# Kernel tuning notes

Hardware: AMD Instinct MI355X
Metric: run time of the kernel (lower is better)

The kernel has to match this reference:

```python
import jax, jax.numpy as jnp
import numpy as np

N, E, D, O, STEP = 100000, 640000, 128, 64, 10


def setup_inputs() -> dict:
    key = jax.random.key(0)
    k1, k2, k3, k4, k5 = jax.random.split(key, 5)
    x = jax.random.normal(k1, (N, D), dtype=jnp.float32)
    edge_index = jax.random.randint(k2, (2, E), 0, N, dtype=jnp.int64)
    t = jax.random.normal(k3, (STEP, D), dtype=jnp.float32)
    W = jax.random.normal(k4, (O, D), dtype=jnp.float32) * 0.05
    b = jax.random.normal(k5, (O,), dtype=jnp.float32) * 0.05
    return {"x": x, "edge_index": edge_index, "t": t, "W": W, "b": b}


def reference(x, edge_index, t, W, b):
    n = x.shape[0]
    # add self loops
    loops = jnp.arange(n, dtype=edge_index.dtype)
    row = jnp.concatenate([edge_index[0], loops])  # source (x_j)
    col = jnp.concatenate([edge_index[1], loops])  # target (aggregation index)
    # symmetric normalization: deg computed over col (targets)
    deg = jax.ops.segment_sum(jnp.ones_like(row, dtype=x.dtype), col, num_segments=n)
    dinv = deg ** -0.5  # deg >= 1 thanks to self loops
    norm = (dinv[row] * dinv[col])[:, None]  # [E+N, 1]
    # per-channel softmax over the 10 hop weights
    t_norm = jax.nn.softmax(t, axis=0)  # [STEP, D]

    def hop(carry, tk):
        h, y = carry
        h = jax.ops.segment_sum(norm * h[row], col, num_segments=n)  # SpMM hop
        return (h, y + tk * h), None

    (_, y), _ = jax.lax.scan(hop, (x, t_norm[0] * x), t_norm[1:])
    return y @ W.T + b
```

## Files before the change

### kernel.cpp

```cpp
#include <hip/hip_runtime.h>

typedef _Float16 half2_t __attribute__((ext_vector_type(2)));
typedef unsigned int uint;

#define D 128
#define O 64
#define UNR 8

static inline size_t align_up(size_t x, size_t a) { return (x + a - 1) & ~(a - 1); }

__device__ __forceinline__ uint pack_f16(float a, float b) {
  half2_t h;
  h.x = (_Float16)a;
  h.y = (_Float16)b;
  return *(uint*)&h;
}

__device__ __forceinline__ float dot2f(uint a, uint b, float c) {
#if defined(__has_builtin) && __has_builtin(__builtin_amdgcn_fdot2)
  return __builtin_amdgcn_fdot2(*(half2_t*)&a, *(half2_t*)&b, c, false);
#else
  half2_t ha = *(half2_t*)&a, hb = *(half2_t*)&b;
  return c + (float)ha.x * (float)hb.x + (float)ha.y * (float)hb.y;
#endif
}


__global__ void count_deg_k(const int* __restrict__ col, int* __restrict__ deg, int E, int n) {
  int i = blockIdx.x * blockDim.x + threadIdx.x;
  if (i >= E) return;
  int c = col[i];
  if ((unsigned)c >= (unsigned)n) return;
  atomicAdd(&deg[c], 1);
}

__global__ void scan1_k(const int* __restrict__ deg, int* __restrict__ row_ptr,
                        int* __restrict__ bsum, float* __restrict__ dinv, int n) {
  __shared__ int s[256];
  int tid = threadIdx.x;
  int gid = blockIdx.x * 256 + tid;
  int dg = (gid < n) ? deg[gid] : 0;
  if (gid < n) dinv[gid] = rsqrtf((float)(dg + 1));
  s[tid] = dg;
  __syncthreads();
  for (int off = 1; off < 256; off <<= 1) {
    int t = (tid >= off) ? s[tid - off] : 0;
    __syncthreads();
    s[tid] += t;
    __syncthreads();
  }
  if (gid < n) row_ptr[gid] = s[tid] - dg;
  if (tid == 255) bsum[blockIdx.x] = s[255];
}

__global__ void scan2_k(int* __restrict__ bsum, int nb) {
  __shared__ int s[512];
  int tid = threadIdx.x;
  int v = (tid < nb) ? bsum[tid] : 0;
  s[tid] = v;
  __syncthreads();
  for (int off = 1; off < 512; off <<= 1) {
    int t = (tid >= off) ? s[tid - off] : 0;
    __syncthreads();
    s[tid] += t;
    __syncthreads();
  }
  if (tid < nb) bsum[tid] = s[tid] - v;
}

__global__ void scan3_k(const int* __restrict__ bsum, const int* __restrict__ deg,
                        int* __restrict__ row_ptr, int* __restrict__ cursor, int n) {
  int gid = blockIdx.x * 256 + threadIdx.x;
  if (gid < n) {
    int r = row_ptr[gid] + bsum[blockIdx.x];
    row_ptr[gid] = r;
    cursor[gid] = r;
    if (gid == n - 1) row_ptr[n] = r + deg[gid];
  }
}

__global__ void fill_k(const int* __restrict__ rows, const int* __restrict__ cols,
                       int* __restrict__ cursor, const float* __restrict__ dinv,
                       int2* __restrict__ csr, int E, int n) {
  int i = blockIdx.x * blockDim.x + threadIdx.x;
  if (i >= E) return;
  int u = rows[i], v = cols[i];
  if ((unsigned)v >= (unsigned)n) return;
  if ((unsigned)u >= (unsigned)n) u = 0;
  int slot = atomicAdd(&cursor[v], 1);
  float nrm = dinv[u] * dinv[v];
  csr[slot] = make_int2(u, __float_as_int(nrm));
}

__global__ void prep_k(const float* __restrict__ t, float* __restrict__ tn,
                       const float* __restrict__ W, uint* __restrict__ Wpk, int step) {
  int tid = threadIdx.x;
  if (tid < D) {
    float vals[16];
    float m = -1e30f;
    for (int k = 0; k < step; ++k) { vals[k] = t[k * D + tid]; m = fmaxf(m, vals[k]); }
    float ssum = 0.f;
    for (int k = 0; k < step; ++k) { vals[k] = expf(vals[k] - m); ssum += vals[k]; }
    float inv = 1.f / ssum;
    for (int k = 0; k < step; ++k) tn[k * D + tid] = vals[k] * inv;
  }
  for (int i = tid; i < O * 64; i += 256) {
    int o = i & 63, dd = i >> 6;
    Wpk[i] = pack_f16(W[o * D + 2 * dd], W[o * D + 2 * dd + 1]);
  }
}

__global__ void init_h_k(const float* __restrict__ x, uint* __restrict__ h0, int total) {
  int i = blockIdx.x * blockDim.x + threadIdx.x;
  if (i >= total) return;
  float2 v = ((const float2*)x)[i];
  h0[i] = pack_f16(v.x, v.y);
}


__global__ __launch_bounds__(256) void hop_k(
    const uint* __restrict__ hsrc, uint* __restrict__ hdst,
    const int* __restrict__ row_ptr, const int2* __restrict__ csr,
    const float* __restrict__ dinv, int n) {
  int wid = (blockIdx.x * blockDim.x + threadIdx.x) >> 6;
  int lane = threadIdx.x & 63;
  if (wid >= n) return;
  int v = __builtin_amdgcn_readfirstlane(wid);
  float dv = dinv[v];
  float ns = dv * dv;
  uint hp = hsrc[(size_t)v * 64 + lane];
  half2_t hv = *(half2_t*)&hp;
  float hx = (float)hv.x, hy = (float)hv.y;
  float ax = ns * hx, ay = ns * hy;
  int beg = __builtin_amdgcn_readfirstlane(row_ptr[v]);
  int end = __builtin_amdgcn_readfirstlane(row_ptr[v + 1]);
  for (int i = beg; i < end; i += UNR) {
    int u[UNR];
    float w[UNR];
#pragma unroll
    for (int j = 0; j < UNR; ++j) {
      int ic = i + j;
      int icl = (ic < end - 1) ? ic : (end - 1);
      int2 e = csr[icl];
      u[j] = e.x;
      w[j] = (ic < end) ? __int_as_float(e.y) : 0.f;
    }
    uint g[UNR];
#pragma unroll
    for (int j = 0; j < UNR; ++j) g[j] = hsrc[(size_t)u[j] * 64 + lane];
#pragma unroll
    for (int j = 0; j < UNR; ++j) {
      half2_t h = *(half2_t*)&g[j];
      ax += w[j] * (float)h.x;
      ay += w[j] * (float)h.y;
    }
  }
  hdst[(size_t)v * 64 + lane] = pack_f16(ax, ay);
}


#define PNW 8

template <int STEPT, bool XF16>
__global__ __launch_bounds__(256) void proj_k(
    const float* __restrict__ x, const uint* __restrict__ hbuf, size_t hstride,
    const uint* __restrict__ Wpk, const float* __restrict__ tn,
    const float* __restrict__ b, float* __restrict__ out, int n, int step) {
  __shared__ uint sy[4][64];
  int tid = threadIdx.x;
  int lane = tid & 63, wv = tid >> 6;
  uint wreg[64];
#pragma unroll
  for (int j = 0; j < 64; ++j) wreg[j] = Wpk[j * 64 + lane];
  float bias = b[lane];
  float2 tt[STEPT > 0 ? STEPT : 1];
  if (STEPT > 0) {
#pragma unroll
    for (int k = 0; k < STEPT; ++k) tt[k] = ((const float2*)(tn + (size_t)k * D))[lane];
  }
  int wid = (blockIdx.x * blockDim.x + tid) >> 6;
  int vb = wid * PNW;
  int ve = vb + PNW < n ? vb + PNW : n;
  for (int v = vb; v < ve; ++v) {
    float yx, yy;
    if (STEPT > 0) {
      if (XF16) {
        uint hp = hbuf[(size_t)v * 64 + lane];
        half2_t h = *(half2_t*)&hp;
        yx = tt[0].x * (float)h.x;
        yy = tt[0].y * (float)h.y;
#pragma unroll
        for (int k = 1; k < STEPT; ++k) {
          uint hq = hbuf[(size_t)k * hstride + (size_t)v * 64 + lane];
          half2_t hh = *(half2_t*)&hq;
          yx += tt[k].x * (float)hh.x;
          yy += tt[k].y * (float)hh.y;
        }
      } else {
        float2 xv = ((const float2*)x)[(size_t)v * 64 + lane];
        yx = tt[0].x * xv.x;
        yy = tt[0].y * xv.y;
#pragma unroll
        for (int k = 1; k < STEPT; ++k) {
          uint hq = hbuf[(size_t)(k - 1) * hstride + (size_t)v * 64 + lane];
          half2_t hh = *(half2_t*)&hq;
          yx += tt[k].x * (float)hh.x;
          yy += tt[k].y * (float)hh.y;
        }
      }
    } else {
      float2 t0 = ((const float2*)tn)[lane];
      float2 xv = ((const float2*)x)[(size_t)v * 64 + lane];
      yx = t0.x * xv.x;
      yy = t0.y * xv.y;
      for (int k = 1; k < step; ++k) {
        uint hq = hbuf[(size_t)(k - 1) * hstride + (size_t)v * 64 + lane];
        half2_t hh = *(half2_t*)&hq;
        float2 tk = ((const float2*)(tn + (size_t)k * D))[lane];
        yx += tk.x * (float)hh.x;
        yy += tk.y * (float)hh.y;
      }
    }
    sy[wv][lane] = pack_f16(yx, yy);
    float acc = bias;
#pragma unroll
    for (int q = 0; q < 16; ++q) {
      uint4 yq = *(const uint4*)&sy[wv][q * 4];
      acc = dot2f(yq.x, wreg[q * 4 + 0], acc);
      acc = dot2f(yq.y, wreg[q * 4 + 1], acc);
      acc = dot2f(yq.z, wreg[q * 4 + 2], acc);
      acc = dot2f(yq.w, wreg[q * 4 + 3], acc);
    }
    out[(size_t)v * O + lane] = acc;
  }
}


template <int DO_Y>
__global__ __launch_bounds__(256) void hop_f_k(
    const uint* __restrict__ h_old, uint* __restrict__ h_new, uint* __restrict__ y,
    const int* __restrict__ row_ptr, const int2* __restrict__ csr,
    const float* __restrict__ dinv, const float* __restrict__ tprev,
    const float* __restrict__ tcur, int n) {
  int wid = (blockIdx.x * blockDim.x + threadIdx.x) >> 6;
  int lane = threadIdx.x & 63;
  if (wid >= n) return;
  int v = __builtin_amdgcn_readfirstlane(wid);
  float dv = dinv[v];
  float ns = dv * dv;
  uint hp = h_old[(size_t)v * 64 + lane];
  half2_t hv = *(half2_t*)&hp;
  float hx = (float)hv.x, hy = (float)hv.y;
  float ax = ns * hx, ay = ns * hy;
  int beg = __builtin_amdgcn_readfirstlane(row_ptr[v]);
  int end = __builtin_amdgcn_readfirstlane(row_ptr[v + 1]);
  for (int i = beg; i < end; i += UNR) {
    int u[UNR];
    float w[UNR];
#pragma unroll
    for (int j = 0; j < UNR; ++j) {
      int ic = i + j;
      int icl = (ic < end - 1) ? ic : (end - 1);
      int2 e = csr[icl];
      u[j] = e.x;
      w[j] = (ic < end) ? __int_as_float(e.y) : 0.f;
    }
    uint g[UNR];
#pragma unroll
    for (int j = 0; j < UNR; ++j) g[j] = h_old[(size_t)u[j] * 64 + lane];
#pragma unroll
    for (int j = 0; j < UNR; ++j) {
      half2_t h = *(half2_t*)&g[j];
      ax += w[j] * (float)h.x;
      ay += w[j] * (float)h.y;
    }
  }
  h_new[(size_t)v * 64 + lane] = pack_f16(ax, ay);
  if (DO_Y) {
    float2 ta = ((const float2*)tprev)[lane];
    float2 tb = ((const float2*)tcur)[lane];
    float yx = ta.x * hx + tb.x * ax;
    float yy = ta.y * hy + tb.y * ay;
    if (DO_Y == 2) {
      uint yo = y[(size_t)v * 64 + lane];
      half2_t yh = *(half2_t*)&yo;
      yx += (float)yh.x;
      yy += (float)yh.y;
    }
    y[(size_t)v * 64 + lane] = pack_f16(yx, yy);
  }
}

__global__ __launch_bounds__(256) void proj_y_k(
    const uint* __restrict__ y, const uint* __restrict__ Wpk,
    const float* __restrict__ b, float* __restrict__ out, int n, int nwaves) {
  int lane = threadIdx.x & 63;
  int wid = (blockIdx.x * blockDim.x + threadIdx.x) >> 6;
  uint wreg[64];
#pragma unroll
  for (int j = 0; j < 64; ++j) wreg[j] = Wpk[j * 64 + lane];
  float bias = b[lane];
  for (int v = wid; v < n; v += nwaves) {
    int vu = __builtin_amdgcn_readfirstlane(v);
    const uint* yrow = y + (size_t)vu * 64;
    float acc = bias;
#pragma unroll
    for (int dd = 0; dd < 64; ++dd) acc = dot2f(yrow[dd], wreg[dd], acc);
    out[(size_t)vu * O + lane] = acc;
  }
}


extern "C" void kernel_launch(void* const* d_in, const int* in_sizes, int n_in,
                              void* d_out, int out_size, void* d_ws, size_t ws_size,
                              hipStream_t stream) {
  const float* x = (const float*)d_in[0];
  const int* ei = (const int*)d_in[1];
  const float* t = (const float*)d_in[2];
  const float* W = (const float*)d_in[3];
  const float* b = (const float*)d_in[4];
  float* out = (float*)d_out;

  int n = in_sizes[0] / D;
  int E = in_sizes[1] / 2;
  int step = in_sizes[2] / D;
  const int* rows = ei;
  const int* cols = ei + E;

  char* p = (char*)d_ws;
  auto alloc = [&](size_t bytes) { char* r = p; p += align_up(bytes, 256); return r; };
  int*   deg     = (int*)alloc((size_t)n * 4);
  float* dinv    = (float*)alloc((size_t)n * 4);
  int*   row_ptr = (int*)alloc((size_t)(n + 1) * 4);
  int*   cursor  = (int*)alloc((size_t)n * 4);
  int*   bsum    = (int*)alloc(2048);
  int2*  csr     = (int2*)alloc((size_t)E * 8);
  float* tn      = (float*)alloc((size_t)step * D * 4);
  uint*  Wpk     = (uint*)alloc((size_t)O * 64 * 4);

  size_t NS = (size_t)n * 64;
  size_t base = (size_t)(p - (char*)d_ws);
  bool fullx = (ws_size >= base + (size_t)step * NS * 4) && (step >= 3);
  bool full  = (ws_size >= base + (size_t)(step - 1) * NS * 4) && (step >= 3);

  hipMemsetAsync(deg, 0, (size_t)n * 4, stream);
  int nb1 = (n + 255) / 256;
  count_deg_k<<<(E + 255) / 256, 256, 0, stream>>>(cols, deg, E, n);
  scan1_k<<<nb1, 256, 0, stream>>>(deg, row_ptr, bsum, dinv, n);
  scan2_k<<<1, 512, 0, stream>>>(bsum, nb1);
  scan3_k<<<nb1, 256, 0, stream>>>(bsum, deg, row_ptr, cursor, n);
  fill_k<<<(E + 255) / 256, 256, 0, stream>>>(rows, cols, cursor, dinv, csr, E, n);
  prep_k<<<1, 256, 0, stream>>>(t, tn, W, Wpk, step);

  int hop_blocks = (n + 3) / 4;
  int proj_blocks = (n + PNW * 4 - 1) / (PNW * 4);

  if (fullx) {
    uint* hbuf = (uint*)alloc((size_t)step * NS * 4);
    init_h_k<<<((size_t)NS + 255) / 256, 256, 0, stream>>>(x, hbuf, (int)NS);
    for (int k = 1; k < step; ++k) {
      hop_k<<<hop_blocks, 256, 0, stream>>>(hbuf + (size_t)(k - 1) * NS,
                                            hbuf + (size_t)k * NS, row_ptr, csr, dinv, n);
    }
    if (step == 10)
      proj_k<10, true><<<proj_blocks, 256, 0, stream>>>(x, hbuf, NS, Wpk, tn, b, out, n, step);
    else
      proj_k<0, false><<<proj_blocks, 256, 0, stream>>>(x, hbuf + NS, NS, Wpk, tn, b, out, n, step);
  } else if (full) {
    uint* hbuf = (uint*)alloc((size_t)(step - 1) * NS * 4);
    uint* h0 = hbuf + (size_t)(step - 2) * NS;
    init_h_k<<<((size_t)NS + 255) / 256, 256, 0, stream>>>(x, h0, (int)NS);
    hop_k<<<hop_blocks, 256, 0, stream>>>(h0, hbuf, row_ptr, csr, dinv, n);
    for (int k = 2; k < step; ++k) {
      hop_k<<<hop_blocks, 256, 0, stream>>>(hbuf + (size_t)(k - 2) * NS,
                                            hbuf + (size_t)(k - 1) * NS, row_ptr, csr, dinv, n);
    }
    if (step == 10)
      proj_k<10, false><<<proj_blocks, 256, 0, stream>>>(x, hbuf, NS, Wpk, tn, b, out, n, step);
    else
      proj_k<0, false><<<proj_blocks, 256, 0, stream>>>(x, hbuf, NS, Wpk, tn, b, out, n, step);
  } else {
    uint* h_a  = (uint*)alloc(NS * 4);
    uint* h_b  = (uint*)alloc(NS * 4);
    uint* ybuf = (uint*)alloc(NS * 4);
    init_h_k<<<((size_t)NS + 255) / 256, 256, 0, stream>>>(x, h_a, (int)NS);
    uint* ho = h_a;
    uint* hn = h_b;
    for (int k = 1; k < step; ++k) {
      const float* tp = tn + (size_t)(k - 1) * D;
      const float* tc = tn + (size_t)k * D;
      if (k & 1) {
        if (k == 1)
          hop_f_k<1><<<hop_blocks, 256, 0, stream>>>(ho, hn, ybuf, row_ptr, csr, dinv, tp, tc, n);
        else
          hop_f_k<2><<<hop_blocks, 256, 0, stream>>>(ho, hn, ybuf, row_ptr, csr, dinv, tp, tc, n);
      } else {
        hop_f_k<0><<<hop_blocks, 256, 0, stream>>>(ho, hn, ybuf, row_ptr, csr, dinv, tp, tc, n);
      }
      uint* tmp = ho; ho = hn; hn = tmp;
    }
    proj_y_k<<<512, 256, 0, stream>>>(ybuf, Wpk, b, out, n, 2048);
  }
}
```

Before: 520.5 us.

## Always fuse hop-weighted accumulation into hops; drop store-all-hops projection path

Removes the paths that stored every hop's features in fp16 and later re-read all of them in a separate projection kernel. Every hop now runs through the fused hop kernel, which adds the softmax-weighted terms into a single fp16 y buffer every other hop. A new DO_Y=3 variant covers the final even hop when the step count is odd. The final projection now batches several nodes per wave and broadcasts y through LDS. The aim is to cut the large multi-buffer write and readback and the workspace footprint, at the cost of extra read-modify-write traffic on y inside the hops.

```diff
diff --git a/kernel.cpp b/kernel.cpp
--- a/kernel.cpp
+++ b/kernel.cpp
@@ -115,124 +115,6 @@
   if (i >= total) return;
   float2 v = ((const float2*)x)[i];
   h0[i] = pack_f16(v.x, v.y);
-}
-
-
-__global__ __launch_bounds__(256) void hop_k(
-    const uint* __restrict__ hsrc, uint* __restrict__ hdst,
-    const int* __restrict__ row_ptr, const int2* __restrict__ csr,
-    const float* __restrict__ dinv, int n) {
-  int wid = (blockIdx.x * blockDim.x + threadIdx.x) >> 6;
-  int lane = threadIdx.x & 63;
-  if (wid >= n) return;
-  int v = __builtin_amdgcn_readfirstlane(wid);
-  float dv = dinv[v];
-  float ns = dv * dv;
-  uint hp = hsrc[(size_t)v * 64 + lane];
-  half2_t hv = *(half2_t*)&hp;
-  float hx = (float)hv.x, hy = (float)hv.y;
-  float ax = ns * hx, ay = ns * hy;
-  int beg = __builtin_amdgcn_readfirstlane(row_ptr[v]);
-  int end = __builtin_amdgcn_readfirstlane(row_ptr[v + 1]);
-  for (int i = beg; i < end; i += UNR) {
-    int u[UNR];
-    float w[UNR];
-#pragma unroll
-    for (int j = 0; j < UNR; ++j) {
-      int ic = i + j;
-      int icl = (ic < end - 1) ? ic : (end - 1);
-      int2 e = csr[icl];
-      u[j] = e.x;
-      w[j] = (ic < end) ? __int_as_float(e.y) : 0.f;
-    }
-    uint g[UNR];
-#pragma unroll
-    for (int j = 0; j < UNR; ++j) g[j] = hsrc[(size_t)u[j] * 64 + lane];
-#pragma unroll
-    for (int j = 0; j < UNR; ++j) {
-      half2_t h = *(half2_t*)&g[j];
-      ax += w[j] * (float)h.x;
-      ay += w[j] * (float)h.y;
-    }
-  }
-  hdst[(size_t)v * 64 + lane] = pack_f16(ax, ay);
-}
-
-
-#define PNW 8
-
-template <int STEPT, bool XF16>
-__global__ __launch_bounds__(256) void proj_k(
-    const float* __restrict__ x, const uint* __restrict__ hbuf, size_t hstride,
-    const uint* __restrict__ Wpk, const float* __restrict__ tn,
-    const float* __restrict__ b, float* __restrict__ out, int n, int step) {
-  __shared__ uint sy[4][64];
-  int tid = threadIdx.x;
-  int lane = tid & 63, wv = tid >> 6;
-  uint wreg[64];
-#pragma unroll
-  for (int j = 0; j < 64; ++j) wreg[j] = Wpk[j * 64 + lane];
-  float bias = b[lane];
-  float2 tt[STEPT > 0 ? STEPT : 1];
-  if (STEPT > 0) {
-#pragma unroll
-    for (int k = 0; k < STEPT; ++k) tt[k] = ((const float2*)(tn + (size_t)k * D))[lane];
-  }
-  int wid = (blockIdx.x * blockDim.x + tid) >> 6;
-  int vb = wid * PNW;
-  int ve = vb + PNW < n ? vb + PNW : n;
-  for (int v = vb; v < ve; ++v) {
-    float yx, yy;
-    if (STEPT > 0) {
-      if (XF16) {
-        uint hp = hbuf[(size_t)v * 64 + lane];
-        half2_t h = *(half2_t*)&hp;
-        yx = tt[0].x * (float)h.x;
-        yy = tt[0].y * (float)h.y;
-#pragma unroll
-        for (int k = 1; k < STEPT; ++k) {
-          uint hq = hbuf[(size_t)k * hstride + (size_t)v * 64 + lane];
-          half2_t hh = *(half2_t*)&hq;
-          yx += tt[k].x * (float)hh.x;
-          yy += tt[k].y * (float)hh.y;
-        }
-      } else {
-        float2 xv = ((const float2*)x)[(size_t)v * 64 + lane];
-        yx = tt[0].x * xv.x;
-        yy = tt[0].y * xv.y;
-#pragma unroll
-        for (int k = 1; k < STEPT; ++k) {
-          uint hq = hbuf[(size_t)(k - 1) * hstride + (size_t)v * 64 + lane];
-          half2_t hh = *(half2_t*)&hq;
-          yx += tt[k].x * (float)hh.x;
-          yy += tt[k].y * (float)hh.y;
-        }
-      }
-    } else {
-      float2 t0 = ((const float2*)tn)[lane];
-      float2 xv = ((const float2*)x)[(size_t)v * 64 + lane];
-      yx = t0.x * xv.x;
-      yy = t0.y * xv.y;
-      for (int k = 1; k < step; ++k) {
-        uint hq = hbuf[(size_t)(k - 1) * hstride + (size_t)v * 64 + lane];
-        half2_t hh = *(half2_t*)&hq;
-        float2 tk = ((const float2*)(tn + (size_t)k * D))[lane];
-        yx += tk.x * (float)hh.x;
-        yy += tk.y * (float)hh.y;
-      }
-    }
-    sy[wv][lane] = pack_f16(yx, yy);
-    float acc = bias;
-#pragma unroll
-    for (int q = 0; q < 16; ++q) {
-      uint4 yq = *(const uint4*)&sy[wv][q * 4];
-      acc = dot2f(yq.x, wreg[q * 4 + 0], acc);
-      acc = dot2f(yq.y, wreg[q * 4 + 1], acc);
-      acc = dot2f(yq.z, wreg[q * 4 + 2], acc);
-      acc = dot2f(yq.w, wreg[q * 4 + 3], acc);
-    }
-    out[(size_t)v * O + lane] = acc;
-  }
 }
 
 
@@ -277,11 +159,16 @@
   }
   h_new[(size_t)v * 64 + lane] = pack_f16(ax, ay);
   if (DO_Y) {
-    float2 ta = ((const float2*)tprev)[lane];
+    float yx = 0.f, yy = 0.f;
+    if (DO_Y != 3) {
+      float2 ta = ((const float2*)tprev)[lane];
+      yx = ta.x * hx;
+      yy = ta.y * hy;
+    }
     float2 tb = ((const float2*)tcur)[lane];
-    float yx = ta.x * hx + tb.x * ax;
-    float yy = ta.y * hy + tb.y * ay;
-    if (DO_Y == 2) {
+    yx += tb.x * ax;
+    yy += tb.y * ay;
+    if (DO_Y >= 2) {
       uint yo = y[(size_t)v * 64 + lane];
       half2_t yh = *(half2_t*)&yo;
       yx += (float)yh.x;
@@ -291,22 +178,34 @@
   }
 }
 
-__global__ __launch_bounds__(256) void proj_y_k(
+
+#define PNW 8
+
+__global__ __launch_bounds__(256) void proj_y2_k(
     const uint* __restrict__ y, const uint* __restrict__ Wpk,
-    const float* __restrict__ b, float* __restrict__ out, int n, int nwaves) {
-  int lane = threadIdx.x & 63;
-  int wid = (blockIdx.x * blockDim.x + threadIdx.x) >> 6;
+    const float* __restrict__ b, float* __restrict__ out, int n) {
+  __shared__ uint sy[4][64];
+  int tid = threadIdx.x;
+  int lane = tid & 63, wv = tid >> 6;
   uint wreg[64];
 #pragma unroll
   for (int j = 0; j < 64; ++j) wreg[j] = Wpk[j * 64 + lane];
   float bias = b[lane];
-  for (int v = wid; v < n; v += nwaves) {
-    int vu = __builtin_amdgcn_readfirstlane(v);
-    const uint* yrow = y + (size_t)vu * 64;
+  int wid = (blockIdx.x * blockDim.x + tid) >> 6;
+  int vb = wid * PNW;
+  int ve = vb + PNW < n ? vb + PNW : n;
+  for (int v = vb; v < ve; ++v) {
+    sy[wv][lane] = y[(size_t)v * 64 + lane];
     float acc = bias;
 #pragma unroll
-    for (int dd = 0; dd < 64; ++dd) acc = dot2f(yrow[dd], wreg[dd], acc);
-    out[(size_t)vu * O + lane] = acc;
+    for (int q = 0; q < 16; ++q) {
+      uint4 yq = *(const uint4*)&sy[wv][q * 4];
+      acc = dot2f(yq.x, wreg[q * 4 + 0], acc);
+      acc = dot2f(yq.y, wreg[q * 4 + 1], acc);
+      acc = dot2f(yq.z, wreg[q * 4 + 2], acc);
+      acc = dot2f(yq.w, wreg[q * 4 + 3], acc);
+    }
+    out[(size_t)v * O + lane] = acc;
   }
 }
 
@@ -339,9 +238,9 @@
   uint*  Wpk     = (uint*)alloc((size_t)O * 64 * 4);
 
   size_t NS = (size_t)n * 64;
-  size_t base = (size_t)(p - (char*)d_ws);
-  bool fullx = (ws_size >= base + (size_t)step * NS * 4) && (step >= 3);
-  bool full  = (ws_size >= base + (size_t)(step - 1) * NS * 4) && (step >= 3);
+  uint* h_a  = (uint*)alloc(NS * 4);
+  uint* h_b  = (uint*)alloc(NS * 4);
+  uint* ybuf = (uint*)alloc(NS * 4);
 
   hipMemsetAsync(deg, 0, (size_t)n * 4, stream);
   int nb1 = (n + 255) / 256;
@@ -355,50 +254,24 @@
   int hop_blocks = (n + 3) / 4;
   int proj_blocks = (n + PNW * 4 - 1) / (PNW * 4);
 
-  if (fullx) {
-    uint* hbuf = (uint*)alloc((size_t)step * NS * 4);
-    init_h_k<<<((size_t)NS + 255) / 256, 256, 0, stream>>>(x, hbuf, (int)NS);
-    for (int k = 1; k < step; ++k) {
-      hop_k<<<hop_blocks, 256, 0, stream>>>(hbuf + (size_t)(k - 1) * NS,
-                                            hbuf + (size_t)k * NS, row_ptr, csr, dinv, n);
-    }
-    if (step == 10)
-      proj_k<10, true><<<proj_blocks, 256, 0, stream>>>(x, hbuf, NS, Wpk, tn, b, out, n, step);
-    else
-      proj_k<0, false><<<proj_blocks, 256, 0, stream>>>(x, hbuf + NS, NS, Wpk, tn, b, out, n, step);
-  } else if (full) {
-    uint* hbuf = (uint*)alloc((size_t)(step - 1) * NS * 4);
-    uint* h0 = hbuf + (size_t)(step - 2) * NS;
-    init_h_k<<<((size_t)NS + 255) / 256, 256, 0, stream>>>(x, h0, (int)NS);
-    hop_k<<<hop_blocks, 256, 0, stream>>>(h0, hbuf, row_ptr, csr, dinv, n);
-    for (int k = 2; k < step; ++k) {
-      hop_k<<<hop_blocks, 256, 0, stream>>>(hbuf + (size_t)(k - 2) * NS,
-                                            hbuf + (size_t)(k - 1) * NS, row_ptr, csr, dinv, n);
-    }
-    if (step == 10)
-      proj_k<10, false><<<proj_blocks, 256, 0, stream>>>(x, hbuf, NS, Wpk, tn, b, out, n, step);
-    else
-      proj_k<0, false><<<proj_blocks, 256, 0, stream>>>(x, hbuf, NS, Wpk, tn, b, out, n, step);
-  } else {
-    uint* h_a  = (uint*)alloc(NS * 4);
-    uint* h_b  = (uint*)alloc(NS * 4);
-    uint* ybuf = (uint*)alloc(NS * 4);
-    init_h_k<<<((size_t)NS + 255) / 256, 256, 0, stream>>>(x, h_a, (int)NS);
-    uint* ho = h_a;
-    uint* hn = h_b;
-    for (int k = 1; k < step; ++k) {
-      const float* tp = tn + (size_t)(k - 1) * D;
-      const float* tc = tn + (size_t)k * D;
-      if (k & 1) {
-        if (k == 1)
-          hop_f_k<1><<<hop_blocks, 256, 0, stream>>>(ho, hn, ybuf, row_ptr, csr, dinv, tp, tc, n);
-        else
-          hop_f_k<2><<<hop_blocks, 256, 0, stream>>>(ho, hn, ybuf, row_ptr, csr, dinv, tp, tc, n);
-      } else {
-        hop_f_k<0><<<hop_blocks, 256, 0, stream>>>(ho, hn, ybuf, row_ptr, csr, dinv, tp, tc, n);
-      }
-      uint* tmp = ho; ho = hn; hn = tmp;
-    }
-    proj_y_k<<<512, 256, 0, stream>>>(ybuf, Wpk, b, out, n, 2048);
-  }
-}
+  init_h_k<<<((size_t)NS + 255) / 256, 256, 0, stream>>>(x, h_a, (int)NS);
+  uint* ho = h_a;
+  uint* hn = h_b;
+  for (int k = 1; k < step; ++k) {
+    const float* tp = tn + (size_t)(k - 1) * D;
+    const float* tc = tn + (size_t)k * D;
+    if (k & 1) {
+      if (k == 1)
+        hop_f_k<1><<<hop_blocks, 256, 0, stream>>>(ho, hn, ybuf, row_ptr, csr, dinv, tp, tc, n);
+      else
+        hop_f_k<2><<<hop_blocks, 256, 0, stream>>>(ho, hn, ybuf, row_ptr, csr, dinv, tp, tc, n);
+    } else if (k == step - 1) {
+      hop_f_k<3><<<hop_blocks, 256, 0, stream>>>(ho, hn, ybuf, row_ptr, csr, dinv, tp, tc, n);
+    } else {
+      hop_f_k<0><<<hop_blocks, 256, 0, stream>>>(ho, hn, ybuf, row_ptr, csr, dinv, tp, tc, n);
+    }
+    uint* tmp = ho; ho = hn; hn = tmp;
+  }
+
+  proj_y2_k<<<proj_blocks, 256, 0, stream>>>(ybuf, Wpk, b, out, n);
+}
```

Measured after the change: 526.2 us. No clear change (+1.1%).
